# Optimization experiments

Measured on AMD Instinct MI355X. Metric: run time of the kernel, lower is better.

## Reference

```python
import jax, jax.numpy as jnp
import numpy as np

B, DIM, H, W = 1, 256, 64, 64
NUM_HEADS = 8
N_GROUPS = 4
KK = 9                      # ksizes[blk_ids=0]
KV_H, KV_W = 64, 64         # kv_size[blk_ids=0]
NGC = DIM // N_GROUPS       # n_group_channels = 64
NHC = DIM // NUM_HEADS      # n_head_channels = 32
NGH = NUM_HEADS // N_GROUPS # n_group_heads = 2
OFFSET_RANGE_FACTOR = 2.0
SCALE = NHC ** -0.5
LN_EPS = 1e-5


def setup_inputs() -> dict:
    key = jax.random.key(0)
    ks = jax.random.split(key, 10)
    def n(k, shape, std=0.02):
        return jax.random.normal(k, shape, jnp.float32) * std
    return {
        "x": jax.random.normal(ks[0], (B, DIM, H, W), jnp.float32),
        "wq": n(ks[1], (DIM, DIM)), "bq": jnp.zeros((DIM,), jnp.float32),
        "wk": n(ks[2], (DIM, DIM)), "bk": jnp.zeros((DIM,), jnp.float32),
        "wv": n(ks[3], (DIM, DIM)), "bv": jnp.zeros((DIM,), jnp.float32),
        "w_off_dw": n(ks[4], (NGC, 1, KK, KK)), "b_off_dw": jnp.zeros((NGC,), jnp.float32),
        "ln_g": jnp.ones((NGC,), jnp.float32), "ln_b": jnp.zeros((NGC,), jnp.float32),
        "w_off_pw": n(ks[5], (2, NGC)),
        "rpe_table": n(ks[6], (NUM_HEADS, 2 * KV_H - 1, 2 * KV_W - 1), 0.01),
        "w_out": n(ks[7], (DIM, DIM)), "b_out": jnp.zeros((DIM,), jnp.float32),
    }


def conv1x1(x, w, b=None):
    # x: [B,C,H,W], w: [O,C]
    y = jnp.einsum('bchw,oc->bohw', x, w)
    if b is not None:
        y = y + b[None, :, None, None]
    return y


def grid_sample_bilinear(inp, grid):
    # Faithful F.grid_sample(mode='bilinear', align_corners=True, padding_mode='zeros').
    # inp: [N,C,Hi,Wi], grid: [N,Hg,Wg,2] with (x,y) in [-1,1].
    N, C, Hi, Wi = inp.shape
    gx = (grid[..., 0] + 1.0) * 0.5 * (Wi - 1)
    gy = (grid[..., 1] + 1.0) * 0.5 * (Hi - 1)
    x0 = jnp.floor(gx)
    y0 = jnp.floor(gy)
    gather_b = jax.vmap(lambda im, iy, ix: im[:, iy, ix])  # -> [N,C,Hg,Wg]
    out = jnp.zeros((N, C) + grid.shape[1:3], inp.dtype)
    for dy in (0.0, 1.0):
        for dx in (0.0, 1.0):
            ix = x0 + dx
            iy = y0 + dy
            wgt = (1.0 - jnp.abs(gx - ix)) * (1.0 - jnp.abs(gy - iy))
            valid = (ix >= 0) & (ix <= Wi - 1) & (iy >= 0) & (iy <= Hi - 1)
            ixc = jnp.clip(ix, 0, Wi - 1).astype(jnp.int32)
            iyc = jnp.clip(iy, 0, Hi - 1).astype(jnp.int32)
            out = out + gather_b(inp, iyc, ixc) * (wgt * valid)[:, None]
    return out


def ref_points(Hk, Wk, n):
    # normalized (y, x) reference grid, matching _get_ref_points
    ry = (jnp.arange(Hk, dtype=jnp.float32) + 0.5) / Hk * 2.0 - 1.0
    rx = (jnp.arange(Wk, dtype=jnp.float32) + 0.5) / Wk * 2.0 - 1.0
    ref = jnp.stack(jnp.meshgrid(ry, rx, indexing='ij'), -1)  # [Hk,Wk,2]
    return jnp.broadcast_to(ref[None], (n, Hk, Wk, 2))


def reference(x, wq, bq, wk, bk, wv, bv, w_off_dw, b_off_dw, ln_g, ln_b,
              w_off_pw, rpe_table, w_out, b_out):
    Bx, C, Hx, Wx = x.shape
    q = conv1x1(x, wq, bq)
    q_off = q.reshape(Bx * N_GROUPS, NGC, Hx, Wx)

    # conv_offset: depthwise conv -> LayerNorm(channels) -> GELU -> 1x1 conv (no bias)
    o = jax.lax.conv_general_dilated(
        q_off, w_off_dw, window_strides=(1, 1),
        padding=[(KK // 2, KK // 2), (KK // 2, KK // 2)],
        feature_group_count=NGC,
        dimension_numbers=('NCHW', 'OIHW', 'NCHW'))
    o = o + b_off_dw[None, :, None, None]
    mu = o.mean(1, keepdims=True)
    var = o.var(1, keepdims=True)
    o = (o - mu) / jnp.sqrt(var + LN_EPS) * ln_g[None, :, None, None] + ln_b[None, :, None, None]
    o = jax.nn.gelu(o, approximate=False)
    offset = jnp.einsum('bchw,oc->bohw', o, w_off_pw)  # [B*g, 2, Hk, Wk]

    Hk, Wk = offset.shape[2], offset.shape[3]
    n_sample = Hk * Wk
    off_range = jnp.array([1.0 / Hk, 1.0 / Wk], jnp.float32).reshape(1, 2, 1, 1)
    offset = jnp.tanh(offset) * off_range * OFFSET_RANGE_FACTOR
    offset = offset.transpose(0, 2, 3, 1)  # [B*g, Hk, Wk, 2] (y, x)

    pos = offset + ref_points(Hk, Wk, Bx * N_GROUPS)

    x_g = x.reshape(Bx * N_GROUPS, NGC, Hx, Wx)
    x_sampled = grid_sample_bilinear(x_g, pos[..., ::-1])  # grid is (x, y)
    x_sampled = x_sampled.reshape(Bx, C, 1, n_sample)

    qf = q.reshape(Bx * NUM_HEADS, NHC, Hx * Wx)
    k = conv1x1(x_sampled, wk, bk).reshape(Bx * NUM_HEADS, NHC, n_sample)
    v = conv1x1(x_sampled, wv, bv).reshape(Bx * NUM_HEADS, NHC, n_sample)

    attn = jnp.einsum('bcm,bcn->bmn', qf, k) * SCALE  # [B*h, HW, n_sample]

    # RPE bias via bilinear sampling of rpe_table at displacement grid
    q_grid = ref_points(Hx, Wx, Bx * N_GROUPS)
    disp = (q_grid.reshape(Bx * N_GROUPS, Hx * Wx, 1, 2)
            - pos.reshape(Bx * N_GROUPS, 1, n_sample, 2)) * 0.5
    rpe = jnp.broadcast_to(rpe_table[None], (Bx,) + rpe_table.shape)
    rpe = rpe.reshape(Bx * N_GROUPS, NGH, 2 * Hx - 1, 2 * Wx - 1)
    attn_bias = grid_sample_bilinear(rpe, disp[..., ::-1])
    attn_bias = attn_bias.reshape(Bx * NUM_HEADS, Hx * Wx, n_sample)

    attn = jax.nn.softmax(attn + attn_bias, axis=2)
    out = jnp.einsum('bmn,bcn->bcm', attn, v).reshape(Bx, C, Hx, Wx)
    return conv1x1(out, w_out, b_out)
```

## Files before the change

kernel.cpp:

```cpp
#include <hip/hip_runtime.h>
#include <hip/hip_bf16.h>
#include <math.h>

#define HW 4096
#define SCALE 0.17677669529663687f
#define LOG2E 1.4426950408889634f

typedef __attribute__((ext_vector_type(8))) short short8;
typedef __attribute__((ext_vector_type(4))) float f32x4;
typedef __attribute__((ext_vector_type(4))) unsigned int u32x4;
typedef __attribute__((ext_vector_type(2))) unsigned int u32x2;
typedef __attribute__((ext_vector_type(2), aligned(8))) unsigned int u32x2a;

static __device__ __forceinline__ unsigned short bf16b(float f) {
  __hip_bfloat16 h = __float2bfloat16(f);
  return *reinterpret_cast<unsigned short*>(&h);
}

__global__ __launch_bounds__(256) void gemm256(const float* __restrict__ W,
                                               const float* __restrict__ bias,
                                               const float* __restrict__ X,
                                               float* __restrict__ Yf,
                                               unsigned short* __restrict__ Yt,
                                               float sc) {
  int tid = threadIdx.x;
  int o0 = (blockIdx.x >> 3) * 8;
  int p = (blockIdx.x & 7) * 512 + tid * 2;
  const float* Wb = W + o0 * 256;
  float ax[8], ay[8];
  #pragma unroll
  for (int i = 0; i < 8; ++i) { ax[i] = 0.f; ay[i] = 0.f; }
  #pragma unroll 4
  for (int c = 0; c < 256; ++c) {
    float2 xv = *(const float2*)(X + c * HW + p);
    #pragma unroll
    for (int i = 0; i < 8; ++i) {
      float wv = Wb[i * 256 + c];
      ax[i] += wv * xv.x;
      ay[i] += wv * xv.y;
    }
  }
  float rx[8], ry[8];
  #pragma unroll
  for (int i = 0; i < 8; ++i) {
    float b = bias[o0 + i];
    rx[i] = ax[i] + b;
    ry[i] = ay[i] + b;
  }
  if (Yf) {
    #pragma unroll
    for (int i = 0; i < 8; ++i) {
      float2 st = {rx[i], ry[i]};
      *(float2*)(Yf + (size_t)(o0 + i) * HW + p) = st;
    }
  }
  if (Yt) {
    int h = o0 >> 5, c0 = o0 & 31;
    u32x4 pk0, pk1;
    #pragma unroll
    for (int j = 0; j < 4; ++j) {
      pk0[j] = (unsigned int)bf16b(rx[2 * j] * sc) | ((unsigned int)bf16b(rx[2 * j + 1] * sc) << 16);
      pk1[j] = (unsigned int)bf16b(ry[2 * j] * sc) | ((unsigned int)bf16b(ry[2 * j + 1] * sc) << 16);
    }
    *(u32x4*)(Yt + ((size_t)(h * HW + p) * 32 + c0)) = pk0;
    *(u32x4*)(Yt + ((size_t)(h * HW + p + 1) * 32 + c0)) = pk1;
  }
}

__global__ __launch_bounds__(256) void gemm_kv(const float* __restrict__ Wk,
                                               const float* __restrict__ bk,
                                               const float* __restrict__ Wv,
                                               const float* __restrict__ bv,
                                               const float* __restrict__ X,
                                               unsigned short* __restrict__ Yt,
                                               unsigned short* __restrict__ Yv) {
  int tid = threadIdx.x;
  int o0 = (blockIdx.x >> 3) * 8;
  int p = (blockIdx.x & 7) * 512 + tid * 2;
  const float* Wkb = Wk + o0 * 256;
  const float* Wvb = Wv + o0 * 256;
  float kxa[8], kya[8], vxa[8], vya[8];
  #pragma unroll
  for (int i = 0; i < 8; ++i) { kxa[i] = 0.f; kya[i] = 0.f; vxa[i] = 0.f; vya[i] = 0.f; }
  #pragma unroll 2
  for (int c = 0; c < 256; ++c) {
    float2 xv = *(const float2*)(X + c * HW + p);
    #pragma unroll
    for (int i = 0; i < 8; ++i) {
      float wk = Wkb[i * 256 + c];
      float wv = Wvb[i * 256 + c];
      kxa[i] += wk * xv.x;
      kya[i] += wk * xv.y;
      vxa[i] += wv * xv.x;
      vya[i] += wv * xv.y;
    }
  }
  float kx[8], ky[8];
  #pragma unroll
  for (int i = 0; i < 8; ++i) {
    float b = bk[o0 + i];
    kx[i] = kxa[i] + b;
    ky[i] = kya[i] + b;
  }
  {
    int h = o0 >> 5, c0 = o0 & 31;
    u32x4 pk0, pk1;
    #pragma unroll
    for (int j = 0; j < 4; ++j) {
      pk0[j] = (unsigned int)bf16b(kx[2 * j]) | ((unsigned int)bf16b(kx[2 * j + 1]) << 16);
      pk1[j] = (unsigned int)bf16b(ky[2 * j]) | ((unsigned int)bf16b(ky[2 * j + 1]) << 16);
    }
    *(u32x4*)(Yt + ((size_t)(h * HW + p) * 32 + c0)) = pk0;
    *(u32x4*)(Yt + ((size_t)(h * HW + p + 1) * 32 + c0)) = pk1;
  }
  #pragma unroll
  for (int i = 0; i < 8; ++i) {
    float b = bv[o0 + i];
    unsigned int pk = (unsigned int)bf16b(vxa[i] + b) | ((unsigned int)bf16b(vya[i] + b) << 16);
    *(unsigned int*)(Yv + (size_t)(o0 + i) * HW + p) = pk;
  }
}

__global__ __launch_bounds__(256) void dwconv_kernel(const float* __restrict__ q,
                                                     const float* __restrict__ wdw,
                                                     const float* __restrict__ bdw,
                                                     float* __restrict__ o) {
  int x = threadIdx.x & 63;
  int w = threadIdx.x >> 6;
  int bid = blockIdx.x;
  int half = bid & 1; int c = (bid >> 1) & 63; int g = bid >> 7;
  int y0 = half * 32 + w * 8;
  const float* qc = q + (g * 64 + c) * HW;
  const float* wc = wdw + c * 81;
  float b = bdw[c];
  float acc[8];
  #pragma unroll
  for (int i = 0; i < 8; ++i) acc[i] = b;
  #pragma unroll
  for (int r = 0; r < 16; ++r) {
    int yy = y0 - 4 + r;
    bool rowok = (unsigned)yy <= 63u;
    int yc = min(max(yy, 0), 63);
    float v[9];
    #pragma unroll
    for (int kx = 0; kx < 9; ++kx) {
      int xx = x + kx - 4;
      bool ok = rowok && ((unsigned)xx <= 63u);
      int xc = min(max(xx, 0), 63);
      float lv = qc[yc * 64 + xc];
      v[kx] = ok ? lv : 0.f;
    }
    #pragma unroll
    for (int oy = 0; oy < 8; ++oy) {
      int ky = r - oy;
      if (ky < 0 || ky > 8) continue;
      #pragma unroll
      for (int kx = 0; kx < 9; ++kx)
        acc[oy] += wc[ky * 9 + kx] * v[kx];
    }
  }
  #pragma unroll
  for (int oy = 0; oy < 8; ++oy)
    o[(g * 64 + c) * HW + (y0 + oy) * 64 + x] = acc[oy];
}

__global__ __launch_bounds__(256) void ln_offset_kernel(const float* __restrict__ o,
                                                        const float* __restrict__ ln_g,
                                                        const float* __restrict__ ln_b,
                                                        const float* __restrict__ wpw,
                                                        float* __restrict__ pos,
                                                        float* __restrict__ cxy) {
  int wave = threadIdx.x >> 6;
  int c = threadIdx.x & 63;
  int bid = blockIdx.x;
  int xc = bid & 15; int y = (bid >> 4) & 63; int g = bid >> 10;
  int x = xc * 4 + wave;
  int p = y * 64 + x;
  float v = o[(g * 64 + c) * HW + p];
  float s = v, s2 = v * v;
  #pragma unroll
  for (int m = 32; m; m >>= 1) { s += __shfl_xor(s, m); s2 += __shfl_xor(s2, m); }
  float mu = s * (1.f / 64.f);
  float var = s2 * (1.f / 64.f) - mu * mu;
  float nv = (v - mu) * rsqrtf(var + 1e-5f) * ln_g[c] + ln_b[c];
  nv = 0.5f * nv * (1.f + erff(nv * 0.70710678118654752f));
  float t0 = wpw[c] * nv, t1 = wpw[64 + c] * nv;
  #pragma unroll
  for (int m = 32; m; m >>= 1) { t0 += __shfl_xor(t0, m); t1 += __shfl_xor(t1, m); }
  if (c == 0) {
    float offy = tanhf(t0) * (2.0f / 64.0f);
    float offx = tanhf(t1) * (2.0f / 64.0f);
    float py = offy + (y + 0.5f) * (2.f / 64.f) - 1.f;
    float px = offx + (x + 0.5f) * (2.f / 64.f) - 1.f;
    pos[(g * HW + p) * 2 + 0] = py;
    pos[(g * HW + p) * 2 + 1] = px;
    cxy[(g * HW + p) * 2 + 0] = 64.0f - 31.5f * px;
    cxy[(g * HW + p) * 2 + 1] = 64.0f - 31.5f * py;
  }
}

__global__ __launch_bounds__(256) void sample_kernel(const float* __restrict__ x,
                                                     const float* __restrict__ pos,
                                                     float* __restrict__ xs) {
  int bid = blockIdx.x;
  int cc = bid & 3; int nt = (bid >> 2) & 15; int g = bid >> 6;
  int n = nt * 256 + threadIdx.x;
  float py = pos[(g * HW + n) * 2 + 0];
  float px = pos[(g * HW + n) * 2 + 1];
  float gx = (px + 1.f) * 31.5f;
  float gy = (py + 1.f) * 31.5f;
  float xf = floorf(gx), yf = floorf(gy);
  int xi = (int)xf, yi = (int)yf;
  float fx = gx - xf, fy = gy - yf;
  int x0c = min(max(xi, 0), 63), x1c = min(max(xi + 1, 0), 63);
  int y0c = min(max(yi, 0), 63), y1c = min(max(yi + 1, 0), 63);
  float wx0 = ((unsigned)xi <= 63u) ? (1.f - fx) : 0.f;
  float wx1 = ((unsigned)(xi + 1) <= 63u) ? fx : 0.f;
  float wy0 = ((unsigned)yi <= 63u) ? (1.f - fy) : 0.f;
  float wy1 = ((unsigned)(yi + 1) <= 63u) ? fy : 0.f;
  #pragma unroll 4
  for (int ci = 0; ci < 16; ++ci) {
    int c = cc * 16 + ci;
    const float* xp = x + (g * 64 + c) * HW;
    float vsum = wy0 * (wx0 * xp[y0c * 64 + x0c] + wx1 * xp[y0c * 64 + x1c]) +
                 wy1 * (wx0 * xp[y1c * 64 + x0c] + wx1 * xp[y1c * 64 + x1c]);
    xs[(g * 64 + c) * HW + n] = vsum;
  }
}

__global__ __launch_bounds__(256) void build_rpe4_kernel(const float* __restrict__ rpe,
                                                         unsigned int* __restrict__ tab4) {
  int idx = blockIdx.x * 256 + threadIdx.x;
  if (idx >= 8 * 16641) return;
  int h = idx / 16641; int r = idx - h * 16641;
  int y = r / 129, x = r - y * 129;
  const float* tb = rpe + h * 16129;
  auto pad = [&](int yy, int xx) -> float {
    if (yy < 1 || yy > 127 || xx < 1 || xx > 127) return 0.f;
    return tb[(yy - 1) * 127 + (xx - 1)] * LOG2E;
  };
  unsigned int w0 = (unsigned int)bf16b(pad(y, x)) | ((unsigned int)bf16b(pad(y + 1, x)) << 16);
  unsigned int w1 = (unsigned int)bf16b(pad(y, x + 1)) | ((unsigned int)bf16b(pad(y + 1, x + 1)) << 16);
  u32x2 v = {w0, w1};
  *(u32x2*)(tab4 + (size_t)idx * 2) = v;
}

__global__ __launch_bounds__(256, 3) void attn_kernel(const unsigned short* __restrict__ qt,
                                                      const unsigned short* __restrict__ kt,
                                                      const unsigned short* __restrict__ vbuf,
                                                      const float* __restrict__ cxy,
                                                      const unsigned int* __restrict__ tab4,
                                                      float* __restrict__ att) {
  __shared__ __align__(16) unsigned int P_pack[4][16][20];
  __shared__ float red_l[4][16];
  __shared__ float red_acc[4][32][16];

  int tid = threadIdx.x;
  int w = tid >> 6;
  int l = tid & 63;
  int lm = l & 15;
  int lg = l >> 4;
  int h = blockIdx.x >> 8;
  int mt = blockIdx.x & 255;
  int m0 = mt * 16;
  int m = m0 + lm;
  int xm = m & 63, ym = m >> 6;
  float ex = (xm + 0.5f) * (63.0f / 64.0f) - 31.5f;
  float ey = (ym + 0.5f) * (63.0f / 64.0f) - 31.5f;
  const char* tabb = (const char*)tab4 + (size_t)h * 133128;
  const float* cbase = cxy + (size_t)(h >> 1) * HW * 2;

  short8 qf = *(const short8*)(qt + ((size_t)(h * HW + m) * 32 + 8 * lg));

  f32x4 oA = {0.f, 0.f, 0.f, 0.f};
  f32x4 oB = {0.f, 0.f, 0.f, 0.f};
  float l_lane = 0.f;

  float bias[8];
  float2 ccv[8];
  short8 ka, kb, va, vb;

  {
    float2 cc0[8];
    #pragma unroll
    for (int i = 0; i < 8; ++i) {
      int nl = 16 * (i >> 2) + 4 * lg + (i & 3);
      cc0[i] = *(const float2*)(cbase + (size_t)(w * 32 + nl) * 2);
    }
    int n0 = w * 32;
    ka = *(const short8*)(kt + ((size_t)(h * HW + n0 + lm) * 32 + 8 * lg));
    kb = *(const short8*)(kt + ((size_t)(h * HW + n0 + 16 + lm) * 32 + 8 * lg));
    va = *(const short8*)(vbuf + ((size_t)(h * 32 + lm) * HW + n0 + 8 * lg));
    vb = *(const short8*)(vbuf + ((size_t)(h * 32 + 16 + lm) * HW + n0 + 8 * lg));
    u32x2a tv[8];
    float fxs[8], fys[8];
    #pragma unroll
    for (int i = 0; i < 8; ++i) {
      float gx = ex + cc0[i].x, gy = ey + cc0[i].y;
      float xf = floorf(gx), yf = floorf(gy);
      fxs[i] = gx - xf; fys[i] = gy - yf;
      unsigned off = (unsigned)((int)yf * 1032 + ((int)xf << 3));
      tv[i] = *(const u32x2a*)(tabb + off);
    }
    #pragma unroll
    for (int i = 0; i < 8; ++i) {
      int nl = 16 * (i >> 2) + 4 * lg + (i & 3);
      ccv[i] = *(const float2*)(cbase + (size_t)(128 + w * 32 + nl) * 2);
    }
    #pragma unroll
    for (int i = 0; i < 8; ++i) {
      float a00 = __uint_as_float(tv[i][0] << 16);
      float a10 = __uint_as_float(tv[i][0] & 0xffff0000u);
      float a01 = __uint_as_float(tv[i][1] << 16);
      float a11 = __uint_as_float(tv[i][1] & 0xffff0000u);
      float ly0 = a00 + fys[i] * (a10 - a00);
      float ly1 = a01 + fys[i] * (a11 - a01);
      bias[i] = ly0 + fxs[i] * (ly1 - ly0);
    }
  }

  #pragma unroll 2
  for (int it = 0; it < 32; ++it) {
    f32x4 z = {0.f, 0.f, 0.f, 0.f};
    f32x4 s0 = __builtin_amdgcn_mfma_f32_16x16x32_bf16(ka, qf, z, 0, 0, 0);
    f32x4 s1 = __builtin_amdgcn_mfma_f32_16x16x32_bf16(kb, qf, z, 0, 0, 0);

    int n0n = ((it + 1) & 31) * 128 + w * 32;
    short8 kan = *(const short8*)(kt + ((size_t)(h * HW + n0n + lm) * 32 + 8 * lg));
    short8 kbn = *(const short8*)(kt + ((size_t)(h * HW + n0n + 16 + lm) * 32 + 8 * lg));
    short8 van = *(const short8*)(vbuf + ((size_t)(h * 32 + lm) * HW + n0n + 8 * lg));
    short8 vbn = *(const short8*)(vbuf + ((size_t)(h * 32 + 16 + lm) * HW + n0n + 8 * lg));

    u32x2a tv[8];
    float fxs[8], fys[8];
    #pragma unroll
    for (int i = 0; i < 8; ++i) {
      float gx = ex + ccv[i].x, gy = ey + ccv[i].y;
      float xf = floorf(gx), yf = floorf(gy);
      fxs[i] = gx - xf; fys[i] = gy - yf;
      unsigned off = (unsigned)((int)yf * 1032 + ((int)xf << 3));
      tv[i] = *(const u32x2a*)(tabb + off);
    }
    int n0n2 = ((it + 2) & 31) * 128 + w * 32;
    float2 ccn[8];
    #pragma unroll
    for (int i = 0; i < 8; ++i) {
      int nl = 16 * (i >> 2) + 4 * lg + (i & 3);
      ccn[i] = *(const float2*)(cbase + (size_t)(n0n2 + nl) * 2);
    }

    float p[8];
    #pragma unroll
    for (int i = 0; i < 8; ++i) {
      float qk = (i < 4) ? s0[i & 3] : s1[i & 3];
      p[i] = __builtin_amdgcn_exp2f(qk + bias[i]);
    }
    l_lane += ((p[0] + p[1]) + (p[2] + p[3])) + ((p[4] + p[5]) + (p[6] + p[7]));
    unsigned int w0 = (unsigned int)bf16b(p[0]) | ((unsigned int)bf16b(p[1]) << 16);
    unsigned int w1 = (unsigned int)bf16b(p[2]) | ((unsigned int)bf16b(p[3]) << 16);
    unsigned int w2 = (unsigned int)bf16b(p[4]) | ((unsigned int)bf16b(p[5]) << 16);
    unsigned int w3 = (unsigned int)bf16b(p[6]) | ((unsigned int)bf16b(p[7]) << 16);
    u32x2 wa = {w0, w1}, wb = {w2, w3};
    *(u32x2*)&P_pack[w][lm][2 * lg] = wa;
    *(u32x2*)&P_pack[w][lm][8 + 2 * lg] = wb;
    u32x4 pw = *(u32x4*)&P_pack[w][lm][4 * lg];
    union { u32x4 u; short8 s; } cv; cv.u = pw;
    oA = __builtin_amdgcn_mfma_f32_16x16x32_bf16(va, cv.s, oA, 0, 0, 0);
    oB = __builtin_amdgcn_mfma_f32_16x16x32_bf16(vb, cv.s, oB, 0, 0, 0);

    #pragma unroll
    for (int i = 0; i < 8; ++i) {
      float a00 = __uint_as_float(tv[i][0] << 16);
      float a10 = __uint_as_float(tv[i][0] & 0xffff0000u);
      float a01 = __uint_as_float(tv[i][1] << 16);
      float a11 = __uint_as_float(tv[i][1] & 0xffff0000u);
      float ly0 = a00 + fys[i] * (a10 - a00);
      float ly1 = a01 + fys[i] * (a11 - a01);
      bias[i] = ly0 + fxs[i] * (ly1 - ly0);
    }
    ka = kan; kb = kbn; va = van; vb = vbn;
    #pragma unroll
    for (int i = 0; i < 8; ++i) ccv[i] = ccn[i];
  }

  l_lane += __shfl_xor(l_lane, 16);
  l_lane += __shfl_xor(l_lane, 32);
  if (lg == 0) red_l[w][lm] = l_lane;
  #pragma unroll
  for (int r = 0; r < 4; ++r) {
    red_acc[w][4 * lg + r][lm] = oA[r];
    red_acc[w][16 + 4 * lg + r][lm] = oB[r];
  }
  __syncthreads();
  #pragma unroll
  for (int rep = 0; rep < 2; ++rep) {
    int idx = tid + rep * 256;
    int cl = idx >> 4, mm = idx & 15;
    float lsum = 0.f, osum = 0.f;
    #pragma unroll
    for (int ww = 0; ww < 4; ++ww) {
      lsum += red_l[ww][mm];
      osum += red_acc[ww][cl][mm];
    }
    att[(size_t)(h * 32 + cl) * HW + m0 + mm] = osum / lsum;
  }
}

extern "C" void kernel_launch(void* const* d_in, const int* in_sizes, int n_in,
                              void* d_out, int out_size, void* d_ws, size_t ws_size,
                              hipStream_t stream) {
  const float* x    = (const float*)d_in[0];
  const float* wq   = (const float*)d_in[1];
  const float* bq   = (const float*)d_in[2];
  const float* wk   = (const float*)d_in[3];
  const float* bk   = (const float*)d_in[4];
  const float* wv   = (const float*)d_in[5];
  const float* bv   = (const float*)d_in[6];
  const float* wdw  = (const float*)d_in[7];
  const float* bdw  = (const float*)d_in[8];
  const float* lng  = (const float*)d_in[9];
  const float* lnb  = (const float*)d_in[10];
  const float* wpw  = (const float*)d_in[11];
  const float* rpe  = (const float*)d_in[12];
  const float* wout = (const float*)d_in[13];
  const float* bout = (const float*)d_in[14];
  float* out = (float*)d_out;

  float* ws = (float*)d_ws;
  float* q_f32 = ws;
  float* o_f32 = ws + (1 << 20);
  unsigned short* qt  = (unsigned short*)(ws + (2 << 20));
  unsigned short* ktp = (unsigned short*)(ws + ((2 << 20) + (1 << 19)));
  unsigned short* vbp = (unsigned short*)(ws + (3 << 20));
  float* pos  = ws + ((3 << 20) + (1 << 19));
  float* cxy  = pos + 32768;
  unsigned int* tab4 = (unsigned int*)(cxy + 32768);

  gemm256<<<256, 256, 0, stream>>>(wq, bq, x, q_f32, qt, SCALE * LOG2E);
  build_rpe4_kernel<<<521, 256, 0, stream>>>(rpe, tab4);
  dwconv_kernel<<<512, 256, 0, stream>>>(q_f32, wdw, bdw, o_f32);
  ln_offset_kernel<<<4096, 256, 0, stream>>>(o_f32, lng, lnb, wpw, pos, cxy);
  sample_kernel<<<256, 256, 0, stream>>>(x, pos, q_f32);
  gemm_kv<<<256, 256, 0, stream>>>(wk, bk, wv, bv, q_f32, ktp, vbp);
  attn_kernel<<<2048, 256, 0, stream>>>(qt, ktp, vbp, cxy, tab4, o_f32);
  gemm256<<<256, 256, 0, stream>>>(wout, bout, o_f32, out, nullptr, 1.0f);
}
```

Before: 313.4 us.

## Drop software prefetch in attention loop and load K/V and coords per iteration

Removes the register double-buffering of K/V fragments, sample coordinates and RPE bias, which previously ran one or two iterations ahead. The loop now loads everything for the current tile and computes the bilinear bias inline, with coordinate loads widened to 16-byte vectors. It also drops the min-blocks-per-CU hint from launch_bounds. The aim is to cut register pressure and the prologue code, leaving latency hiding to wave occupancy. The risk is exposed global and table-gather latency inside each iteration.

```diff
diff --git a/kernel.cpp b/kernel.cpp
--- a/kernel.cpp
+++ b/kernel.cpp
@@ -245,12 +245,12 @@
   *(u32x2*)(tab4 + (size_t)idx * 2) = v;
 }
 
-__global__ __launch_bounds__(256, 3) void attn_kernel(const unsigned short* __restrict__ qt,
-                                                      const unsigned short* __restrict__ kt,
-                                                      const unsigned short* __restrict__ vbuf,
-                                                      const float* __restrict__ cxy,
-                                                      const unsigned int* __restrict__ tab4,
-                                                      float* __restrict__ att) {
+__global__ __launch_bounds__(256) void attn_kernel(const unsigned short* __restrict__ qt,
+                                                   const unsigned short* __restrict__ kt,
+                                                   const unsigned short* __restrict__ vbuf,
+                                                   const float* __restrict__ cxy,
+                                                   const unsigned int* __restrict__ tab4,
+                                                   float* __restrict__ att) {
   __shared__ __align__(16) unsigned int P_pack[4][16][20];
   __shared__ float red_l[4][16];
   __shared__ float red_acc[4][32][16];
@@ -276,84 +276,41 @@
   f32x4 oB = {0.f, 0.f, 0.f, 0.f};
   float l_lane = 0.f;
 
-  float bias[8];
-  float2 ccv[8];
-  short8 ka, kb, va, vb;
-
-  {
-    float2 cc0[8];
-    #pragma unroll
-    for (int i = 0; i < 8; ++i) {
-      int nl = 16 * (i >> 2) + 4 * lg + (i & 3);
-      cc0[i] = *(const float2*)(cbase + (size_t)(w * 32 + nl) * 2);
-    }
-    int n0 = w * 32;
-    ka = *(const short8*)(kt + ((size_t)(h * HW + n0 + lm) * 32 + 8 * lg));
-    kb = *(const short8*)(kt + ((size_t)(h * HW + n0 + 16 + lm) * 32 + 8 * lg));
-    va = *(const short8*)(vbuf + ((size_t)(h * 32 + lm) * HW + n0 + 8 * lg));
-    vb = *(const short8*)(vbuf + ((size_t)(h * 32 + 16 + lm) * HW + n0 + 8 * lg));
-    u32x2a tv[8];
-    float fxs[8], fys[8];
-    #pragma unroll
-    for (int i = 0; i < 8; ++i) {
-      float gx = ex + cc0[i].x, gy = ey + cc0[i].y;
-      float xf = floorf(gx), yf = floorf(gy);
-      fxs[i] = gx - xf; fys[i] = gy - yf;
-      unsigned off = (unsigned)((int)yf * 1032 + ((int)xf << 3));
-      tv[i] = *(const u32x2a*)(tabb + off);
-    }
-    #pragma unroll
-    for (int i = 0; i < 8; ++i) {
-      int nl = 16 * (i >> 2) + 4 * lg + (i & 3);
-      ccv[i] = *(const float2*)(cbase + (size_t)(128 + w * 32 + nl) * 2);
-    }
-    #pragma unroll
-    for (int i = 0; i < 8; ++i) {
-      float a00 = __uint_as_float(tv[i][0] << 16);
-      float a10 = __uint_as_float(tv[i][0] & 0xffff0000u);
-      float a01 = __uint_as_float(tv[i][1] << 16);
-      float a11 = __uint_as_float(tv[i][1] & 0xffff0000u);
-      float ly0 = a00 + fys[i] * (a10 - a00);
-      float ly1 = a01 + fys[i] * (a11 - a01);
-      bias[i] = ly0 + fxs[i] * (ly1 - ly0);
-    }
-  }
-
   #pragma unroll 2
   for (int it = 0; it < 32; ++it) {
+    int n0 = (it * 4 + w) * 32;
+    short8 ka = *(const short8*)(kt + ((size_t)(h * HW + n0 + lm) * 32 + 8 * lg));
+    short8 kb = *(const short8*)(kt + ((size_t)(h * HW + n0 + 16 + lm) * 32 + 8 * lg));
+    short8 va = *(const short8*)(vbuf + ((size_t)(h * 32 + lm) * HW + n0 + 8 * lg));
+    short8 vb = *(const short8*)(vbuf + ((size_t)(h * 32 + 16 + lm) * HW + n0 + 8 * lg));
     f32x4 z = {0.f, 0.f, 0.f, 0.f};
     f32x4 s0 = __builtin_amdgcn_mfma_f32_16x16x32_bf16(ka, qf, z, 0, 0, 0);
     f32x4 s1 = __builtin_amdgcn_mfma_f32_16x16x32_bf16(kb, qf, z, 0, 0, 0);
 
-    int n0n = ((it + 1) & 31) * 128 + w * 32;
-    short8 kan = *(const short8*)(kt + ((size_t)(h * HW + n0n + lm) * 32 + 8 * lg));
-    short8 kbn = *(const short8*)(kt + ((size_t)(h * HW + n0n + 16 + lm) * 32 + 8 * lg));
-    short8 van = *(const short8*)(vbuf + ((size_t)(h * 32 + lm) * HW + n0n + 8 * lg));
-    short8 vbn = *(const short8*)(vbuf + ((size_t)(h * 32 + 16 + lm) * HW + n0n + 8 * lg));
-
-    u32x2a tv[8];
-    float fxs[8], fys[8];
+    f32x4 cv[4];
+    cv[0] = *(const f32x4*)(cbase + (size_t)(n0 + 4 * lg) * 2);
+    cv[1] = *(const f32x4*)(cbase + (size_t)(n0 + 4 * lg + 2) * 2);
+    cv[2] = *(const f32x4*)(cbase + (size_t)(n0 + 16 + 4 * lg) * 2);
+    cv[3] = *(const f32x4*)(cbase + (size_t)(n0 + 16 + 4 * lg + 2) * 2);
+
+    float p[8];
     #pragma unroll
     for (int i = 0; i < 8; ++i) {
-      float gx = ex + ccv[i].x, gy = ey + ccv[i].y;
+      float cx = cv[i >> 1][(i & 1) * 2];
+      float cy = cv[i >> 1][(i & 1) * 2 + 1];
+      float gx = ex + cx, gy = ey + cy;
       float xf = floorf(gx), yf = floorf(gy);
-      fxs[i] = gx - xf; fys[i] = gy - yf;
+      float fx = gx - xf, fy = gy - yf;
       unsigned off = (unsigned)((int)yf * 1032 + ((int)xf << 3));
-      tv[i] = *(const u32x2a*)(tabb + off);
-    }
-    int n0n2 = ((it + 2) & 31) * 128 + w * 32;
-    float2 ccn[8];
-    #pragma unroll
-    for (int i = 0; i < 8; ++i) {
-      int nl = 16 * (i >> 2) + 4 * lg + (i & 3);
-      ccn[i] = *(const float2*)(cbase + (size_t)(n0n2 + nl) * 2);
-    }
-
-    float p[8];
-    #pragma unroll
-    for (int i = 0; i < 8; ++i) {
+      u32x2a tv = *(const u32x2a*)(tabb + off);
+      float a00 = __uint_as_float(tv[0] << 16);
+      float a10 = __uint_as_float(tv[0] & 0xffff0000u);
+      float a01 = __uint_as_float(tv[1] << 16);
+      float a11 = __uint_as_float(tv[1] & 0xffff0000u);
+      float ly0 = a00 + fy * (a10 - a00);
+      float ly1 = a01 + fy * (a11 - a01);
       float qk = (i < 4) ? s0[i & 3] : s1[i & 3];
-      p[i] = __builtin_amdgcn_exp2f(qk + bias[i]);
+      p[i] = __builtin_amdgcn_exp2f(qk + (ly0 + fx * (ly1 - ly0)));
     }
     l_lane += ((p[0] + p[1]) + (p[2] + p[3])) + ((p[4] + p[5]) + (p[6] + p[7]));
     unsigned int w0 = (unsigned int)bf16b(p[0]) | ((unsigned int)bf16b(p[1]) << 16);
@@ -364,23 +321,9 @@
     *(u32x2*)&P_pack[w][lm][2 * lg] = wa;
     *(u32x2*)&P_pack[w][lm][8 + 2 * lg] = wb;
     u32x4 pw = *(u32x4*)&P_pack[w][lm][4 * lg];
-    union { u32x4 u; short8 s; } cv; cv.u = pw;
-    oA = __builtin_amdgcn_mfma_f32_16x16x32_bf16(va, cv.s, oA, 0, 0, 0);
-    oB = __builtin_amdgcn_mfma_f32_16x16x32_bf16(vb, cv.s, oB, 0, 0, 0);
-
-    #pragma unroll
-    for (int i = 0; i < 8; ++i) {
-      float a00 = __uint_as_float(tv[i][0] << 16);
-      float a10 = __uint_as_float(tv[i][0] & 0xffff0000u);
-      float a01 = __uint_as_float(tv[i][1] << 16);
-      float a11 = __uint_as_float(tv[i][1] & 0xffff0000u);
-      float ly0 = a00 + fys[i] * (a10 - a00);
-      float ly1 = a01 + fys[i] * (a11 - a01);
-      bias[i] = ly0 + fxs[i] * (ly1 - ly0);
-    }
-    ka = kan; kb = kbn; va = van; vb = vbn;
-    #pragma unroll
-    for (int i = 0; i < 8; ++i) ccv[i] = ccn[i];
+    union { u32x4 u; short8 s; } cvu; cvu.u = pw;
+    oA = __builtin_amdgcn_mfma_f32_16x16x32_bf16(va, cvu.s, oA, 0, 0, 0);
+    oB = __builtin_amdgcn_mfma_f32_16x16x32_bf16(vb, cvu.s, oB, 0, 0, 0);
   }
 
   l_lane += __shfl_xor(l_lane, 16);
```

After: 340.7 us. 8.7% more time.
